# Optimization experiments

Measured on AMD Instinct MI355X. Metric: run time of the kernel, lower is better.

## Reference

```python
import jax, jax.numpy as jnp
import numpy as np

B, S, D, H, E, K = 2, 1024, 1024, 512, 16, 4  # batch, seq, hidden, expert inter, n_experts, top_k
HS = 2 * H  # shared expert inter dim = num_shared_experts * moe_inter_dim


def silu(z):
    return z * jax.nn.sigmoid(z)


def setup_inputs() -> dict:
    key = jax.random.key(0)
    ks = jax.random.split(key, 8)
    sc = lambda fan_in: 1.0 / np.sqrt(fan_in)
    x = jax.random.normal(ks[0], (B, S, D), jnp.float32)
    gate_w = jax.random.normal(ks[1], (E, D), jnp.float32) * sc(D)
    ws_in = jax.random.normal(ks[2], (D, HS), jnp.float32) * sc(D)
    vs_in = jax.random.normal(ks[3], (D, HS), jnp.float32) * sc(D)
    ws_out = jax.random.normal(ks[4], (HS, D), jnp.float32) * sc(HS)
    e_win = jax.random.normal(ks[5], (E, D, H), jnp.float32) * sc(D)
    e_vin = jax.random.normal(ks[6], (E, D, H), jnp.float32) * sc(D)
    e_wout = jax.random.normal(ks[7], (E, H, D), jnp.float32) * sc(H)
    return {"x": x, "gate_w": gate_w, "ws_in": ws_in, "vs_in": vs_in,
            "ws_out": ws_out, "e_win": e_win, "e_vin": e_vin, "e_wout": e_wout}


def reference(x, gate_w, ws_in, vs_in, ws_out, e_win, e_vin, e_wout):
    b, s, d = x.shape
    T = b * s
    xf = x.reshape(T, d)

    # --- Gate (eval path: biases buffer is zero / unused) ---
    g = jax.nn.sigmoid(xf @ gate_w.T)                      # [T, E]
    topv, topi = jax.lax.top_k(g, K)                        # [T, K]
    wn = topv / jnp.sum(topv, axis=-1, keepdims=True)       # normalized top-k weights
    # sparse combine matrix [T, E]: zero for unrouted experts -> exact same math
    # as the original per-expert masked gather/scatter loop
    combine = jnp.zeros_like(g).at[jnp.arange(T)[:, None], topi].add(wn)

    # --- Routed experts (SwiGLU), batched over experts ---
    hin = jnp.einsum('td,edh->eth', xf, e_win)              # [E, T, H]
    vin = jnp.einsum('td,edh->eth', xf, e_vin)              # [E, T, H]
    h = silu(hin) * vin * combine.T[:, :, None]             # weight before down-proj
    routed = jnp.einsum('eth,ehd->td', h, e_wout)           # [T, D]

    # --- Shared expert (SwiGLU with inter = num_shared * moe_inter) ---
    shared = (silu(xf @ ws_in) * (xf @ vs_in)) @ ws_out     # [T, D]

    return (shared + routed).reshape(b, s, d)
```

## Files before the change

### kernel.cpp

```cpp
#include <hip/hip_runtime.h>
#include <hip/hip_bf16.h>
#include <math.h>

typedef __attribute__((ext_vector_type(4))) float f32x4;
typedef __attribute__((ext_vector_type(8))) short s16x8;
typedef __hip_bfloat16 bf16;

constexpr int TOK = 2048;
constexpr int DIM = 1024;
constexpr int HID = 512;
constexpr int NE  = 16;
constexpr int NK  = 4;
constexpr int NHS = 1024;
constexpr int NPAIR = TOK * NK;

constexpr int UP_GRID = 256 + 8 * 80;
constexpr int DN_GRID = 128 + 8 * 80;

#define MFMA(a, b, c) __builtin_amdgcn_mfma_f32_16x16x32_bf16(a, b, c, 0, 0, 0)

#define GLOAD_LDS(gp, lp)                                                        \
  __builtin_amdgcn_global_load_lds(                                              \
      (const __attribute__((address_space(1))) unsigned int*)(gp),               \
      (__attribute__((address_space(3))) unsigned int*)(lp), 16, 0, 0)

template <int CH>
static __device__ __forceinline__ void stage_p(const bf16* const* rp, int k0,
                                               bf16* lds, int tid) {
  int wid = tid >> 6;
#pragma unroll
  for (int i = 0; i < CH; ++i) {
    int c = i * 512 + tid;
    int row = c >> 3;
    int slot = c & 7;
    int j = slot ^ (row & 7);
    const bf16* g = rp[i] + k0 + j * 8;
    bf16* l = lds + (size_t)(i * 512 + wid * 64) * 8;
    GLOAD_LDS(g, l);
  }
}

static __device__ __forceinline__ s16x8 frag(const bf16* lds, int row, int kc) {
  return *(const s16x8*)(lds + row * 64 + ((kc ^ (row & 7)) << 3));
}

static __device__ __forceinline__ float b2f(short u) {
  union { unsigned int i; float f; } c;
  c.i = ((unsigned int)(unsigned short)u) << 16;
  return c.f;
}

struct bf16x4 { bf16 a, b, c, d; };
struct alignas(16) bf16x8 { bf16 v[8]; };


static __device__ __forceinline__ void tr64(const float* __restrict__ src,
                                            bf16* __restrict__ dst, int R, int C,
                                            int bx, int by, float (*t)[65], int tid) {
  int r0 = by * 64, c0 = bx * 64;
#pragma unroll
  for (int i = 0; i < 4; ++i) {
    int row = i * 16 + (tid >> 4);
    int col = (tid & 15) * 4;
    float4 v = *(const float4*)(src + (size_t)(r0 + row) * C + c0 + col);
    t[row][col] = v.x; t[row][col + 1] = v.y;
    t[row][col + 2] = v.z; t[row][col + 3] = v.w;
  }
  __syncthreads();
  int c = tid >> 2;
  int rb = (tid & 3) * 16;
  bf16x8 o0, o1;
#pragma unroll
  for (int k = 0; k < 8; ++k) o0.v[k] = __float2bfloat16(t[rb + k][c]);
#pragma unroll
  for (int k = 0; k < 8; ++k) o1.v[k] = __float2bfloat16(t[rb + 8 + k][c]);
  bf16* d = dst + (size_t)(c0 + c) * R + r0 + rb;
  *(bf16x8*)d = o0;
  *(bf16x8*)(d + 8) = o1;
}

__global__ __launch_bounds__(256) void prep1(const float* __restrict__ ws_in,
                                             const float* __restrict__ vs_in,
                                             const float* __restrict__ e_win,
                                             const float* __restrict__ e_vin,
                                             bf16* __restrict__ wsinT, bf16* __restrict__ vsinT,
                                             bf16* __restrict__ ewinT, bf16* __restrict__ evinT) {
  __shared__ float t[64][65];
  int bid = blockIdx.x, tid = threadIdx.x;
  if (bid < 256) {
    tr64(ws_in, wsinT, DIM, NHS, bid & 15, bid >> 4, t, tid);
  } else if (bid < 512) {
    int b = bid - 256;
    tr64(vs_in, vsinT, DIM, NHS, b & 15, b >> 4, t, tid);
  } else if (bid < 2560) {
    int b = bid - 512, e = b >> 7; b &= 127;
    tr64(e_win + (size_t)e * DIM * HID, ewinT + (size_t)e * DIM * HID,
         DIM, HID, b & 7, b >> 3, t, tid);
  } else {
    int b = bid - 2560, e = b >> 7; b &= 127;
    tr64(e_vin + (size_t)e * DIM * HID, evinT + (size_t)e * DIM * HID,
         DIM, HID, b & 7, b >> 3, t, tid);
  }
}

__global__ __launch_bounds__(256) void prep2(const float* __restrict__ ws_out,
                                             const float* __restrict__ e_wout,
                                             bf16* __restrict__ wsoutT,
                                             bf16* __restrict__ ewoutT) {
  __shared__ float t[64][65];
  int bid = blockIdx.x, tid = threadIdx.x;
  if (bid < 256) {
    tr64(ws_out, wsoutT, NHS, DIM, bid & 15, bid >> 4, t, tid);
  } else {
    int b = bid - 256, e = b >> 7; b &= 127;
    tr64(e_wout + (size_t)e * HID * DIM, ewoutT + (size_t)e * HID * DIM,
         HID, DIM, b & 15, b >> 4, t, tid);
  }
}


__global__ __launch_bounds__(256) void gate_scores(const float* __restrict__ x,
                                                   const float* __restrict__ gw,
                                                   bf16* __restrict__ xb,
                                                   float* __restrict__ scores) {
  int lane = threadIdx.x & 63, wid = threadIdx.x >> 6;
  int t = blockIdx.x * 4 + wid;
  const float* xr = x + (size_t)t * DIM + lane * 16;
  float4 x4[4];
#pragma unroll
  for (int q = 0; q < 4; ++q) x4[q] = *(const float4*)(xr + q * 4);
  {
    bf16* xo = xb + (size_t)t * DIM + lane * 16;
#pragma unroll
    for (int q = 0; q < 4; ++q) {
      bf16x4 o{__float2bfloat16(x4[q].x), __float2bfloat16(x4[q].y),
               __float2bfloat16(x4[q].z), __float2bfloat16(x4[q].w)};
      *reinterpret_cast<bf16x4*>(xo + q * 4) = o;
    }
  }
  float s[NE];
#pragma unroll
  for (int e = 0; e < NE; ++e) {
    const float* wr_ = gw + (size_t)e * DIM + lane * 16;
    float a = 0.f;
#pragma unroll
    for (int q = 0; q < 4; ++q) {
      float4 w4 = *(const float4*)(wr_ + q * 4);
      a += x4[q].x * w4.x + x4[q].y * w4.y + x4[q].z * w4.z + x4[q].w * w4.w;
    }
    s[e] = a;
  }
#pragma unroll
  for (int e = 0; e < NE; ++e)
#pragma unroll
    for (int off = 32; off; off >>= 1) s[e] += __shfl_xor(s[e], off);
  if (lane == 0) {
#pragma unroll
    for (int e = 0; e < NE; ++e) scores[(size_t)t * NE + e] = s[e];
  }
}

__global__ __launch_bounds__(256) void topk_hist(const float* __restrict__ scores,
                                                 int* __restrict__ topi,
                                                 float* __restrict__ topw,
                                                 int* __restrict__ counts) {
  __shared__ int h[NE];
  int tid = threadIdx.x;
  int t = blockIdx.x * 256 + tid;
  if (tid < NE) h[tid] = 0;
  __syncthreads();
  float g[NE];
  const float* sr = scores + (size_t)t * NE;
#pragma unroll
  for (int q = 0; q < 4; ++q) {
    float4 v = *(const float4*)(sr + q * 4);
    g[q * 4 + 0] = 1.f / (1.f + expf(-v.x));
    g[q * 4 + 1] = 1.f / (1.f + expf(-v.y));
    g[q * 4 + 2] = 1.f / (1.f + expf(-v.z));
    g[q * 4 + 3] = 1.f / (1.f + expf(-v.w));
  }
  unsigned used = 0;
  int bi[NK]; float bv[NK];
  float sum = 0.f;
#pragma unroll
  for (int j = 0; j < NK; ++j) {
    int best = 0; float v = -1e30f;
#pragma unroll
    for (int e = 0; e < NE; ++e)
      if (!((used >> e) & 1u) && g[e] > v) { v = g[e]; best = e; }
    used |= 1u << best; bi[j] = best; bv[j] = v; sum += v;
  }
  float inv = 1.f / sum;
#pragma unroll
  for (int j = 0; j < NK; ++j) {
    topi[t * NK + j] = bi[j];
    topw[t * NK + j] = bv[j] * inv;
    atomicAdd(&h[bi[j]], 1);
  }
  __syncthreads();
  if (tid < NE) atomicAdd(&counts[tid], h[tid]);
}

__global__ __launch_bounds__(64) void route_small(const int* __restrict__ counts,
                                                  int* __restrict__ offs,
                                                  int* __restrict__ segs,
                                                  int* __restrict__ nseg,
                                                  int* __restrict__ cursor) {
  if (threadIdx.x != 0) return;
  int o = 0;
#pragma unroll
  for (int e = 0; e < NE; ++e) { offs[e] = o; cursor[e * 32] = 0; o += counts[e]; }
  int s = 0;
  for (int e = 0; e < NE; ++e)
    for (int m = 0; m < counts[e]; m += 128) segs[s++] = (e << 16) | m;
  nseg[0] = s;
}

__global__ __launch_bounds__(256) void scatter_pairs(const int* __restrict__ topi,
                                                     const float* __restrict__ topw,
                                                     const int* __restrict__ offs,
                                                     int* __restrict__ cursor,
                                                     int* __restrict__ tok_list,
                                                     float* __restrict__ w_list,
                                                     int* __restrict__ pair_slot) {
  int p = blockIdx.x * 256 + threadIdx.x;
  if (p >= NPAIR) return;
  int e = topi[p];
  int rank = atomicAdd(&cursor[e * 32], 1);
  int slot = offs[e] + rank;
  tok_list[slot] = p >> 2;
  w_list[slot] = topw[p];
  pair_slot[p] = slot;
}


__global__ __launch_bounds__(512, 4) void up_all(
    const bf16* __restrict__ xb, const bf16* __restrict__ wsinT,
    const bf16* __restrict__ vsinT, const bf16* __restrict__ ewinT,
    const bf16* __restrict__ evinT, const int* __restrict__ tok_list,
    const float* __restrict__ w_list, const int* __restrict__ counts,
    const int* __restrict__ offs, const int* __restrict__ segs,
    const int* __restrict__ nseg, bf16* __restrict__ hsb,
    bf16* __restrict__ hre) {
  int bid = blockIdx.x;
  int j = (bid & 7) * (UP_GRID / 8) + (bid >> 3);
  int nj = 256 + 8 * nseg[0];
  if (j >= nj) return;
  int tid = threadIdx.x, lane = tid & 63, wid = tid >> 6;
  int wr = wid >> 2, wc = wid & 3;

  bool is_shared = (j < 256);
  int m0, n0, cnt = TOK, off_e = 0;
  const bf16 *w1, *w2;
  if (is_shared) {
    m0 = (j >> 4) * 128; n0 = j & 15;
    w1 = wsinT; w2 = vsinT;
  } else {
    int r = j - 256;
    int sv = segs[r >> 3]; n0 = r & 7;
    int e = sv >> 16; m0 = sv & 0xffff;
    cnt = counts[e]; off_e = offs[e];
    w1 = ewinT + (size_t)e * HID * DIM;
    w2 = evinT + (size_t)e * HID * DIM;
  }

  const bf16* ap[2]; const bf16* bp[2];
#pragma unroll
  for (int i = 0; i < 2; ++i) {
    int row = (i * 512 + tid) >> 3;
    int gr = is_shared ? (m0 + row) : tok_list[off_e + min(m0 + row, cnt - 1)];
    ap[i] = xb + (size_t)gr * DIM;
  }
#pragma unroll
  for (int i = 0; i < 2; ++i) {
    int r = (i * 512 + tid) >> 3;
    int ridx = n0 * 64 + (r >> 5) * 16 + (r & 15);
    bp[i] = ((r & 16) ? w2 : w1) + (size_t)ridx * DIM;
  }

  __shared__ alignas(16) bf16 As[2][128 * 64], Bs[2][128 * 64];
  f32x4 acc[4][2];
  f32x4 z4 = {0.f, 0.f, 0.f, 0.f};
#pragma unroll
  for (int m = 0; m < 4; ++m) { acc[m][0] = z4; acc[m][1] = z4; }

  constexpr int NT = DIM / 64;
  stage_p<2>(ap, 0, As[0], tid);
  stage_p<2>(bp, 0, Bs[0], tid);
  stage_p<2>(ap, 64, As[1], tid);
  stage_p<2>(bp, 64, Bs[1], tid);

  for (int kt = 0; kt < NT; ++kt) {
    int cur = kt & 1;
    if (kt + 1 < NT) asm volatile("s_waitcnt vmcnt(4)" ::: "memory");
    else             asm volatile("s_waitcnt vmcnt(0)" ::: "memory");
    __builtin_amdgcn_sched_barrier(0);
    __builtin_amdgcn_s_barrier();
    __builtin_amdgcn_sched_barrier(0);
    const bf16* Ac = As[cur]; const bf16* Bc = Bs[cur];
    __builtin_amdgcn_s_setprio(1);
#pragma unroll
    for (int ks = 0; ks < 2; ++ks) {
      int r16 = lane & 15, kc = (ks << 2) + (lane >> 4);
      s16x8 a[4];
#pragma unroll
      for (int m = 0; m < 4; ++m) a[m] = frag(Ac, wr * 64 + m * 16 + r16, kc);
#pragma unroll
      for (int q = 0; q < 2; ++q) {
        s16x8 b = frag(Bc, wc * 32 + q * 16 + r16, kc);
#pragma unroll
        for (int m = 0; m < 4; ++m) acc[m][q] = MFMA(a[m], b, acc[m][q]);
      }
    }
    __builtin_amdgcn_s_setprio(0);
    __builtin_amdgcn_s_barrier();
    __builtin_amdgcn_sched_barrier(0);
    if (kt + 2 < NT) {
      stage_p<2>(ap, (kt + 2) * 64, As[cur], tid);
      stage_p<2>(bp, (kt + 2) * 64, Bs[cur], tid);
    }
  }

  int c = n0 * 64 + wc * 16 + (lane & 15);
#pragma unroll
  for (int m = 0; m < 4; ++m)
#pragma unroll
    for (int i = 0; i < 4; ++i) {
      int r = wr * 64 + m * 16 + (lane >> 4) * 4 + i;
      float z = acc[m][0][i], v = acc[m][1][i];
      float h = z / (1.f + __expf(-z)) * v;
      if (is_shared) {
        hsb[(size_t)(m0 + r) * NHS + c] = __float2bfloat16(h);
      } else {
        int gr = m0 + r;
        if (gr < cnt)
          hre[(size_t)(off_e + gr) * HID + c] =
              __float2bfloat16(h * w_list[off_e + gr]);
      }
    }
}


__global__ __launch_bounds__(512, 4) void down_all(
    const bf16* __restrict__ hsb, const bf16* __restrict__ wsoutT,
    const bf16* __restrict__ hre, const bf16* __restrict__ ewoutT,
    const int* __restrict__ tok_list, const int* __restrict__ counts,
    const int* __restrict__ offs, const int* __restrict__ segs,
    const int* __restrict__ nseg, float* __restrict__ out,
    bf16* __restrict__ hrd) {
  int bid = blockIdx.x;
  int j = (bid & 7) * (DN_GRID / 8) + (bid >> 3);
  int nj = 128 + 8 * nseg[0];
  if (j >= nj) return;
  int tid = threadIdx.x, lane = tid & 63, wid = tid >> 6;
  int wr = wid >> 2, wc = wid & 3;

  bool is_shared = (j < 128);
  int m0, n0, cnt = TOK, off_e = 0, K, ldA, ldB;
  const bf16 *Abase, *Bbase;
  if (is_shared) {
    m0 = (j >> 3) * 128; n0 = j & 7;
    Abase = hsb; ldA = NHS; K = NHS;
    Bbase = wsoutT; ldB = NHS;
  } else {
    int r = j - 128;
    int sv = segs[r >> 3]; n0 = r & 7;
    int e = sv >> 16; m0 = sv & 0xffff;
    cnt = counts[e]; off_e = offs[e];
    Abase = hre + (size_t)off_e * HID; ldA = HID; K = HID;
    Bbase = ewoutT + (size_t)e * DIM * HID; ldB = HID;
  }

  const bf16* ap[2]; const bf16* bp[2];
#pragma unroll
  for (int i = 0; i < 2; ++i) {
    int row = (i * 512 + tid) >> 3;
    int gr = is_shared ? (m0 + row) : min(m0 + row, cnt - 1);
    ap[i] = Abase + (size_t)gr * ldA;
  }
#pragma unroll
  for (int i = 0; i < 2; ++i) {
    int r = (i * 512 + tid) >> 3;
    bp[i] = Bbase + (size_t)(n0 * 128 + r) * ldB;
  }

  __shared__ alignas(16) bf16 As[2][128 * 64], Bs[2][128 * 64];
  f32x4 acc[4][2];
  f32x4 z4 = {0.f, 0.f, 0.f, 0.f};
#pragma unroll
  for (int m = 0; m < 4; ++m) { acc[m][0] = z4; acc[m][1] = z4; }

  int NT = K / 64;
  stage_p<2>(ap, 0, As[0], tid);
  stage_p<2>(bp, 0, Bs[0], tid);
  stage_p<2>(ap, 64, As[1], tid);
  stage_p<2>(bp, 64, Bs[1], tid);

  for (int kt = 0; kt < NT; ++kt) {
    int cur = kt & 1;
    if (kt + 1 < NT) asm volatile("s_waitcnt vmcnt(4)" ::: "memory");
    else             asm volatile("s_waitcnt vmcnt(0)" ::: "memory");
    __builtin_amdgcn_sched_barrier(0);
    __builtin_amdgcn_s_barrier();
    __builtin_amdgcn_sched_barrier(0);
    const bf16* Ac = As[cur]; const bf16* Bc = Bs[cur];
    __builtin_amdgcn_s_setprio(1);
#pragma unroll
    for (int ks = 0; ks < 2; ++ks) {
      int r16 = lane & 15, kc = (ks << 2) + (lane >> 4);
      s16x8 a[4];
#pragma unroll
      for (int m = 0; m < 4; ++m) a[m] = frag(Ac, wr * 64 + m * 16 + r16, kc);
#pragma unroll
      for (int q = 0; q < 2; ++q) {
        s16x8 b = frag(Bc, wc * 32 + q * 16 + r16, kc);
#pragma unroll
        for (int m = 0; m < 4; ++m) acc[m][q] = MFMA(a[m], b, acc[m][q]);
      }
    }
    __builtin_amdgcn_s_setprio(0);
    __builtin_amdgcn_s_barrier();
    __builtin_amdgcn_sched_barrier(0);
    if (kt + 2 < NT) {
      stage_p<2>(ap, (kt + 2) * 64, As[cur], tid);
      stage_p<2>(bp, (kt + 2) * 64, Bs[cur], tid);
    }
  }

#pragma unroll
  for (int q = 0; q < 2; ++q) {
    int c = n0 * 128 + wc * 32 + q * 16 + (lane & 15);
#pragma unroll
    for (int m = 0; m < 4; ++m)
#pragma unroll
      for (int i = 0; i < 4; ++i) {
        int r = wr * 64 + m * 16 + (lane >> 4) * 4 + i;
        if (is_shared) {
          out[(size_t)(m0 + r) * DIM + c] = acc[m][q][i];
        } else {
          int gr = m0 + r;
          if (gr < cnt)
            hrd[(size_t)(off_e + gr) * DIM + c] = __float2bfloat16(acc[m][q][i]);
        }
      }
  }
}


__global__ __launch_bounds__(256) void finish_add(const bf16* __restrict__ hrd,
                                                  const int* __restrict__ pair_slot,
                                                  float* __restrict__ out) {
  int idx = blockIdx.x * 256 + threadIdx.x;
  int t = idx >> 7;
  int c0 = (idx & 127) * 8;
  int4 s4 = *(const int4*)(pair_slot + t * 4);
  float acc[8];
  float* o = out + (size_t)t * DIM + c0;
#pragma unroll
  for (int k = 0; k < 8; ++k) acc[k] = o[k];
  int sl[4] = {s4.x, s4.y, s4.z, s4.w};
#pragma unroll
  for (int j = 0; j < 4; ++j) {
    s16x8 v = *(const s16x8*)(hrd + (size_t)sl[j] * DIM + c0);
#pragma unroll
    for (int k = 0; k < 8; ++k) acc[k] += b2f(v[k]);
  }
#pragma unroll
  for (int k = 0; k < 8; ++k) o[k] = acc[k];
}


extern "C" void kernel_launch(void* const* d_in, const int* in_sizes, int n_in,
                              void* d_out, int out_size, void* d_ws, size_t ws_size,
                              hipStream_t stream) {
  const float* x      = (const float*)d_in[0];
  const float* gw     = (const float*)d_in[1];
  const float* ws_in  = (const float*)d_in[2];
  const float* vs_in  = (const float*)d_in[3];
  const float* ws_out = (const float*)d_in[4];
  const float* e_win  = (const float*)d_in[5];
  const float* e_vin  = (const float*)d_in[6];
  const float* e_wout = (const float*)d_in[7];
  float* out = (float*)d_out;

  char* p = (char*)d_ws;
  bf16* xb     = (bf16*)p;  p += (size_t)TOK * DIM * 2;
  bf16* wsinT  = (bf16*)p;
  bf16* wsoutT = wsinT;
  p += (size_t)NHS * DIM * 2;
  bf16* vsinT  = (bf16*)p;  p += (size_t)NHS * DIM * 2;
  bf16* hsb    = (bf16*)p;  p += (size_t)TOK * NHS * 2;
  bf16* ewinT  = (bf16*)p;
  bf16* ewoutT = ewinT;
  p += (size_t)NE * DIM * HID * 2;
  bf16* evinT  = (bf16*)p;
  bf16* hrd    = evinT;
  p += (size_t)NE * DIM * HID * 2;
  bf16* hre    = (bf16*)p;  p += (size_t)(NPAIR + 128) * HID * 2;
  int*   topi      = (int*)p;    p += (size_t)NPAIR * 4;
  float* topw      = (float*)p;  p += (size_t)NPAIR * 4;
  int*   tok_list  = (int*)p;    p += (size_t)NPAIR * 4;
  float* w_list    = (float*)p;  p += (size_t)NPAIR * 4;
  int*   pair_slot = (int*)p;    p += (size_t)NPAIR * 4;
  float* scores    = (float*)p;  p += (size_t)TOK * NE * 4;
  int*   counts    = (int*)p;    p += 64;
  int*   offs      = (int*)p;    p += 64;
  int*   cursor    = (int*)p;    p += NE * 32 * 4;
  int*   segs      = (int*)p;    p += 128 * 4;
  int*   nseg      = (int*)p;    p += 64;

  hipMemsetAsync(counts, 0, NE * sizeof(int), stream);
  gate_scores<<<TOK / 4, 256, 0, stream>>>(x, gw, xb, scores);
  topk_hist<<<TOK / 256, 256, 0, stream>>>(scores, topi, topw, counts);
  route_small<<<1, 64, 0, stream>>>(counts, offs, segs, nseg, cursor);
  scatter_pairs<<<NPAIR / 256, 256, 0, stream>>>(topi, topw, offs, cursor,
                                                 tok_list, w_list, pair_slot);

  prep1<<<4608, 256, 0, stream>>>(ws_in, vs_in, e_win, e_vin,
                                  wsinT, vsinT, ewinT, evinT);

  up_all<<<UP_GRID, 512, 0, stream>>>(xb, wsinT, vsinT, ewinT, evinT, tok_list,
                                      w_list, counts, offs, segs, nseg, hsb, hre);

  prep2<<<2304, 256, 0, stream>>>(ws_out, e_wout, wsoutT, ewoutT);

  down_all<<<DN_GRID, 512, 0, stream>>>(hsb, wsoutT, hre, ewoutT, tok_list,
                                        counts, offs, segs, nseg, out, hrd);
  finish_add<<<TOK * DIM / 8 / 256, 256, 0, stream>>>(hrd, pair_slot, out);
}
```

Measured before the change: 158.6 us.

## Fuse gate scoring into weight-transpose kernel and drop GEMM double buffering

Merges the gate-score/x-to-bf16 kernel into the first weight-transpose prep kernel as extra leading blocks, removing one launch. Separately replaces the double-buffered, waitcnt-pipelined K loop in both up and down GEMMs with a single-buffer load-sync-compute loop. This halves LDS use, which may allow more blocks per CU, but loses the overlap of global loads with MFMA work.

```diff
diff --git a/kernel.cpp b/kernel.cpp
--- a/kernel.cpp
+++ b/kernel.cpp
@@ -79,25 +79,64 @@
   *(bf16x8*)(d + 8) = o1;
 }
 
-__global__ __launch_bounds__(256) void prep1(const float* __restrict__ ws_in,
-                                             const float* __restrict__ vs_in,
-                                             const float* __restrict__ e_win,
-                                             const float* __restrict__ e_vin,
-                                             bf16* __restrict__ wsinT, bf16* __restrict__ vsinT,
-                                             bf16* __restrict__ ewinT, bf16* __restrict__ evinT) {
+
+__global__ __launch_bounds__(256) void prep1_gate(
+    const float* __restrict__ x, const float* __restrict__ gw,
+    bf16* __restrict__ xb, float* __restrict__ scores,
+    const float* __restrict__ ws_in, const float* __restrict__ vs_in,
+    const float* __restrict__ e_win, const float* __restrict__ e_vin,
+    bf16* __restrict__ wsinT, bf16* __restrict__ vsinT,
+    bf16* __restrict__ ewinT, bf16* __restrict__ evinT) {
   __shared__ float t[64][65];
   int bid = blockIdx.x, tid = threadIdx.x;
-  if (bid < 256) {
-    tr64(ws_in, wsinT, DIM, NHS, bid & 15, bid >> 4, t, tid);
-  } else if (bid < 512) {
-    int b = bid - 256;
+  if (bid < 512) {
+    int lane = tid & 63, wid = tid >> 6;
+    int tok = bid * 4 + wid;
+    const float* xr = x + (size_t)tok * DIM + lane * 16;
+    float4 x4[4];
+#pragma unroll
+    for (int q = 0; q < 4; ++q) x4[q] = *(const float4*)(xr + q * 4);
+    bf16* xo = xb + (size_t)tok * DIM + lane * 16;
+#pragma unroll
+    for (int q = 0; q < 4; ++q) {
+      bf16x4 o{__float2bfloat16(x4[q].x), __float2bfloat16(x4[q].y),
+               __float2bfloat16(x4[q].z), __float2bfloat16(x4[q].w)};
+      *reinterpret_cast<bf16x4*>(xo + q * 4) = o;
+    }
+    float s[NE];
+#pragma unroll
+    for (int e = 0; e < NE; ++e) {
+      const float* wr_ = gw + (size_t)e * DIM + lane * 16;
+      float a = 0.f;
+#pragma unroll
+      for (int q = 0; q < 4; ++q) {
+        float4 w4 = *(const float4*)(wr_ + q * 4);
+        a += x4[q].x * w4.x + x4[q].y * w4.y + x4[q].z * w4.z + x4[q].w * w4.w;
+      }
+      s[e] = a;
+    }
+#pragma unroll
+    for (int e = 0; e < NE; ++e)
+#pragma unroll
+      for (int off = 32; off; off >>= 1) s[e] += __shfl_xor(s[e], off);
+    if (lane == 0) {
+#pragma unroll
+      for (int e = 0; e < NE; ++e) scores[(size_t)tok * NE + e] = s[e];
+    }
+    return;
+  }
+  int b0 = bid - 512;
+  if (b0 < 256) {
+    tr64(ws_in, wsinT, DIM, NHS, b0 & 15, b0 >> 4, t, tid);
+  } else if (b0 < 512) {
+    int b = b0 - 256;
     tr64(vs_in, vsinT, DIM, NHS, b & 15, b >> 4, t, tid);
-  } else if (bid < 2560) {
-    int b = bid - 512, e = b >> 7; b &= 127;
+  } else if (b0 < 2560) {
+    int b = b0 - 512, e = b >> 7; b &= 127;
     tr64(e_win + (size_t)e * DIM * HID, ewinT + (size_t)e * DIM * HID,
          DIM, HID, b & 7, b >> 3, t, tid);
   } else {
-    int b = bid - 2560, e = b >> 7; b &= 127;
+    int b = b0 - 2560, e = b >> 7; b &= 127;
     tr64(e_vin + (size_t)e * DIM * HID, evinT + (size_t)e * DIM * HID,
          DIM, HID, b & 7, b >> 3, t, tid);
   }
@@ -115,48 +154,6 @@
     int b = bid - 256, e = b >> 7; b &= 127;
     tr64(e_wout + (size_t)e * HID * DIM, ewoutT + (size_t)e * HID * DIM,
          HID, DIM, b & 15, b >> 4, t, tid);
-  }
-}
-
-
-__global__ __launch_bounds__(256) void gate_scores(const float* __restrict__ x,
-                                                   const float* __restrict__ gw,
-                                                   bf16* __restrict__ xb,
-                                                   float* __restrict__ scores) {
-  int lane = threadIdx.x & 63, wid = threadIdx.x >> 6;
-  int t = blockIdx.x * 4 + wid;
-  const float* xr = x + (size_t)t * DIM + lane * 16;
-  float4 x4[4];
-#pragma unroll
-  for (int q = 0; q < 4; ++q) x4[q] = *(const float4*)(xr + q * 4);
-  {
-    bf16* xo = xb + (size_t)t * DIM + lane * 16;
-#pragma unroll
-    for (int q = 0; q < 4; ++q) {
-      bf16x4 o{__float2bfloat16(x4[q].x), __float2bfloat16(x4[q].y),
-               __float2bfloat16(x4[q].z), __float2bfloat16(x4[q].w)};
-      *reinterpret_cast<bf16x4*>(xo + q * 4) = o;
-    }
-  }
-  float s[NE];
-#pragma unroll
-  for (int e = 0; e < NE; ++e) {
-    const float* wr_ = gw + (size_t)e * DIM + lane * 16;
-    float a = 0.f;
-#pragma unroll
-    for (int q = 0; q < 4; ++q) {
-      float4 w4 = *(const float4*)(wr_ + q * 4);
-      a += x4[q].x * w4.x + x4[q].y * w4.y + x4[q].z * w4.z + x4[q].w * w4.w;
-    }
-    s[e] = a;
-  }
-#pragma unroll
-  for (int e = 0; e < NE; ++e)
-#pragma unroll
-    for (int off = 32; off; off >>= 1) s[e] += __shfl_xor(s[e], off);
-  if (lane == 0) {
-#pragma unroll
-    for (int e = 0; e < NE; ++e) scores[(size_t)t * NE + e] = s[e];
   }
 }
 
@@ -278,49 +275,31 @@
     bp[i] = ((r & 16) ? w2 : w1) + (size_t)ridx * DIM;
   }
 
-  __shared__ alignas(16) bf16 As[2][128 * 64], Bs[2][128 * 64];
+  __shared__ alignas(16) bf16 As[128 * 64], Bs[128 * 64];
   f32x4 acc[4][2];
   f32x4 z4 = {0.f, 0.f, 0.f, 0.f};
 #pragma unroll
   for (int m = 0; m < 4; ++m) { acc[m][0] = z4; acc[m][1] = z4; }
 
-  constexpr int NT = DIM / 64;
-  stage_p<2>(ap, 0, As[0], tid);
-  stage_p<2>(bp, 0, Bs[0], tid);
-  stage_p<2>(ap, 64, As[1], tid);
-  stage_p<2>(bp, 64, Bs[1], tid);
-
-  for (int kt = 0; kt < NT; ++kt) {
-    int cur = kt & 1;
-    if (kt + 1 < NT) asm volatile("s_waitcnt vmcnt(4)" ::: "memory");
-    else             asm volatile("s_waitcnt vmcnt(0)" ::: "memory");
-    __builtin_amdgcn_sched_barrier(0);
-    __builtin_amdgcn_s_barrier();
-    __builtin_amdgcn_sched_barrier(0);
-    const bf16* Ac = As[cur]; const bf16* Bc = Bs[cur];
-    __builtin_amdgcn_s_setprio(1);
+  for (int k0 = 0; k0 < DIM; k0 += 64) {
+    __syncthreads();
+    stage_p<2>(ap, k0, As, tid);
+    stage_p<2>(bp, k0, Bs, tid);
+    __syncthreads();
 #pragma unroll
     for (int ks = 0; ks < 2; ++ks) {
       int r16 = lane & 15, kc = (ks << 2) + (lane >> 4);
       s16x8 a[4];
 #pragma unroll
-      for (int m = 0; m < 4; ++m) a[m] = frag(Ac, wr * 64 + m * 16 + r16, kc);
+      for (int m = 0; m < 4; ++m) a[m] = frag(As, wr * 64 + m * 16 + r16, kc);
 #pragma unroll
       for (int q = 0; q < 2; ++q) {
-        s16x8 b = frag(Bc, wc * 32 + q * 16 + r16, kc);
+        s16x8 b = frag(Bs, wc * 32 + q * 16 + r16, kc);
 #pragma unroll
         for (int m = 0; m < 4; ++m) acc[m][q] = MFMA(a[m], b, acc[m][q]);
       }
     }
-    __builtin_amdgcn_s_setprio(0);
-    __builtin_amdgcn_s_barrier();
-    __builtin_amdgcn_sched_barrier(0);
-    if (kt + 2 < NT) {
-      stage_p<2>(ap, (kt + 2) * 64, As[cur], tid);
-      stage_p<2>(bp, (kt + 2) * 64, Bs[cur], tid);
-    }
-  }
-
+  }
   int c = n0 * 64 + wc * 16 + (lane & 15);
 #pragma unroll
   for (int m = 0; m < 4; ++m)
@@ -384,49 +363,33 @@
     bp[i] = Bbase + (size_t)(n0 * 128 + r) * ldB;
   }
 
-  __shared__ alignas(16) bf16 As[2][128 * 64], Bs[2][128 * 64];
+  __shared__ alignas(16) bf16 As[128 * 64], Bs[128 * 64];
   f32x4 acc[4][2];
   f32x4 z4 = {0.f, 0.f, 0.f, 0.f};
 #pragma unroll
   for (int m = 0; m < 4; ++m) { acc[m][0] = z4; acc[m][1] = z4; }
 
   int NT = K / 64;
-  stage_p<2>(ap, 0, As[0], tid);
-  stage_p<2>(bp, 0, Bs[0], tid);
-  stage_p<2>(ap, 64, As[1], tid);
-  stage_p<2>(bp, 64, Bs[1], tid);
-
   for (int kt = 0; kt < NT; ++kt) {
-    int cur = kt & 1;
-    if (kt + 1 < NT) asm volatile("s_waitcnt vmcnt(4)" ::: "memory");
-    else             asm volatile("s_waitcnt vmcnt(0)" ::: "memory");
-    __builtin_amdgcn_sched_barrier(0);
-    __builtin_amdgcn_s_barrier();
-    __builtin_amdgcn_sched_barrier(0);
-    const bf16* Ac = As[cur]; const bf16* Bc = Bs[cur];
-    __builtin_amdgcn_s_setprio(1);
+    int k0 = kt * 64;
+    __syncthreads();
+    stage_p<2>(ap, k0, As, tid);
+    stage_p<2>(bp, k0, Bs, tid);
+    __syncthreads();
 #pragma unroll
     for (int ks = 0; ks < 2; ++ks) {
       int r16 = lane & 15, kc = (ks << 2) + (lane >> 4);
       s16x8 a[4];
 #pragma unroll
-      for (int m = 0; m < 4; ++m) a[m] = frag(Ac, wr * 64 + m * 16 + r16, kc);
+      for (int m = 0; m < 4; ++m) a[m] = frag(As, wr * 64 + m * 16 + r16, kc);
 #pragma unroll
       for (int q = 0; q < 2; ++q) {
-        s16x8 b = frag(Bc, wc * 32 + q * 16 + r16, kc);
+        s16x8 b = frag(Bs, wc * 32 + q * 16 + r16, kc);
 #pragma unroll
         for (int m = 0; m < 4; ++m) acc[m][q] = MFMA(a[m], b, acc[m][q]);
       }
     }
-    __builtin_amdgcn_s_setprio(0);
-    __builtin_amdgcn_s_barrier();
-    __builtin_amdgcn_sched_barrier(0);
-    if (kt + 2 < NT) {
-      stage_p<2>(ap, (kt + 2) * 64, As[cur], tid);
-      stage_p<2>(bp, (kt + 2) * 64, Bs[cur], tid);
-    }
-  }
-
+  }
 #pragma unroll
   for (int q = 0; q < 2; ++q) {
     int c = n0 * 128 + wc * 32 + q * 16 + (lane & 15);
@@ -510,15 +473,13 @@
   int*   nseg      = (int*)p;    p += 64;
 
   hipMemsetAsync(counts, 0, NE * sizeof(int), stream);
-  gate_scores<<<TOK / 4, 256, 0, stream>>>(x, gw, xb, scores);
+  prep1_gate<<<5120, 256, 0, stream>>>(x, gw, xb, scores, ws_in, vs_in,
+                                       e_win, e_vin, wsinT, vsinT, ewinT, evinT);
   topk_hist<<<TOK / 256, 256, 0, stream>>>(scores, topi, topw, counts);
   route_small<<<1, 64, 0, stream>>>(counts, offs, segs, nseg, cursor);
   scatter_pairs<<<NPAIR / 256, 256, 0, stream>>>(topi, topw, offs, cursor,
                                                  tok_list, w_list, pair_slot);
 
-  prep1<<<4608, 256, 0, stream>>>(ws_in, vs_in, e_win, e_vin,
-                                  wsinT, vsinT, ewinT, evinT);
-
   up_all<<<UP_GRID, 512, 0, stream>>>(xb, wsinT, vsinT, ewinT, evinT, tok_list,
                                       w_list, counts, offs, segs, nseg, hsb, hre);
 
```

Result: faster. 143.7 us (-9.4%).
